# Kernel optimization log

Hardware: AMD Instinct MI355X
Metric: run time of the kernel (lower is better)

## Reference

```python
import jax, jax.numpy as jnp
import numpy as np

# Bit-slice configuration from the module defaults: slices [1,1,2,4] -> 8-bit signed INT.
# The crossbar engine's MapReduceDot decomposes the quantized integers into bit-planes,
# runs partial dot products per (input-slice, weight-slice) pair across paral_size
# partitions, and recombines them with 2^shift weights. In the ideal (noise-free)
# engine this recombination is EXACT, so the forward math equals:
#   dequant(blockwise_quant(x)) @ dequant(blockwise_quant(W^T)) + bias
# with per-block scales determined by the quant granularities.
IN_BITS = 1 + 1 + 2 + 4   # sum(input_slice)  = 8
W_BITS = 1 + 1 + 2 + 4    # sum(weight_slice) = 8
IN_GRAN = (1, 32)         # (rows, cols) blocks over (seq, in_features)
W_GRAN = (32, 32)         # blocks over (in_features, out_features) of weight.t()


def block_fake_quant(x, bits, gran):
    """Symmetric per-block fake quantization (quantize -> dequantize).

    x: [..., R, C]; gran=(gr, gc) tiles the last two dims. Each (gr, gc) block
    gets its own max-abs scale, matching SlicedData's quant_gran semantics.
    """
    qmax = float(2 ** (bits - 1) - 1)  # 127 for 8-bit
    gr, gc = gran
    lead = x.shape[:-2]
    R, C = x.shape[-2], x.shape[-1]
    xb = x.reshape(*lead, R // gr, gr, C // gc, gc)
    mx = jnp.max(jnp.abs(xb), axis=(-3, -1), keepdims=True)
    scale = jnp.where(mx > 0, mx / qmax, jnp.ones_like(mx))
    q = jnp.clip(jnp.round(xb / scale), -qmax, qmax) * scale
    return q.reshape(x.shape)


def setup_inputs() -> dict:
    key = jax.random.key(0)
    k1, k2, k3 = jax.random.split(key, 3)
    B, S, Din, Dout = 4, 4096, 2048, 2048
    x = jax.random.normal(k1, (B, S, Din), dtype=jnp.float32)
    # kaiming_uniform_(a=sqrt(5)) on a Linear weight is U(-1/sqrt(fan_in), 1/sqrt(fan_in))
    bound = 1.0 / np.sqrt(Din)
    weight = jax.random.uniform(k2, (Dout, Din), jnp.float32, -bound, bound)
    bias = jax.random.uniform(k3, (Dout,), jnp.float32, -bound, bound)
    return {"x": x, "weight": weight, "bias": bias}


def reference(x, weight, bias):
    # Quantize activations per (1, 32) block and weight.t() per (32, 32) block,
    # then recombine via the (mathematically exact) bit-sliced dot == dense GEMM
    # on the dequantized values.
    qx = block_fake_quant(x, IN_BITS, IN_GRAN)            # [B, S, Din]
    qw = block_fake_quant(weight.T, W_BITS, W_GRAN)       # [Din, Dout]
    out = jnp.einsum('bsd,de->bse', qx, qw) + bias        # [B, S, Dout]
    return out
```

## Files before the change

kernel.cpp:

```cpp
#include <hip/hip_runtime.h>
#include <hip/hip_bf16.h>
#include <stdint.h>

#define M_TOT 16384
#define N_TOT 2048
#define K_TOT 2048
#define NT 32

typedef __attribute__((ext_vector_type(8))) short bf16x8;
typedef __attribute__((ext_vector_type(4))) float f32x4;

__device__ __forceinline__ ushort f32_to_bf16_rne(float f) {
    uint32_t u = __float_as_uint(f);
    uint32_t r = (u + 0x7fffu + ((u >> 16) & 1u)) >> 16;
    return (ushort)r;
}

__device__ __forceinline__ void async_copy16(const void* gptr, void* lptr) {
    __builtin_amdgcn_global_load_lds(
        (const __attribute__((address_space(1))) uint32_t*)gptr,
        (__attribute__((address_space(3))) uint32_t*)lptr,
        16, 0, 0);
}

__global__ void quant_x_kernel(const float* __restrict__ x, ushort* __restrict__ qx) {
    const int tid = blockIdx.x * 256 + threadIdx.x;
    const float4 v = ((const float4*)x)[tid];
    float m = fmaxf(fmaxf(fabsf(v.x), fabsf(v.y)), fmaxf(fabsf(v.z), fabsf(v.w)));
    m = fmaxf(m, __shfl_xor(m, 1));
    m = fmaxf(m, __shfl_xor(m, 2));
    m = fmaxf(m, __shfl_xor(m, 4));
    const float s = (m > 0.f) ? (m / 127.f) : 1.f;
    const float q0 = fminf(fmaxf(rintf(v.x / s), -127.f), 127.f) * s;
    const float q1 = fminf(fmaxf(rintf(v.y / s), -127.f), 127.f) * s;
    const float q2 = fminf(fmaxf(rintf(v.z / s), -127.f), 127.f) * s;
    const float q3 = fminf(fmaxf(rintf(v.w / s), -127.f), 127.f) * s;
    ushort4 r;
    r.x = f32_to_bf16_rne(q0);
    r.y = f32_to_bf16_rne(q1);
    r.z = f32_to_bf16_rne(q2);
    r.w = f32_to_bf16_rne(q3);
    ((ushort4*)qx)[tid] = r;
}

__global__ void quant_w_kernel(const float* __restrict__ w, ushort* __restrict__ qw) {
    const int gtid = blockIdx.x * 256 + threadIdx.x;
    const int wid  = gtid >> 6;
    const int lane = gtid & 63;
    const int tn = wid >> 6;
    const int tk = wid & 63;
    const int row = tn * 32 + (lane >> 1);
    const int col = tk * 32 + ((lane & 1) << 4);
    const float* p = w + (size_t)row * K_TOT + col;
    const float4 v0 = ((const float4*)p)[0];
    const float4 v1 = ((const float4*)p)[1];
    const float4 v2 = ((const float4*)p)[2];
    const float4 v3 = ((const float4*)p)[3];
    float m = 0.f;
#define MAX4(V) m = fmaxf(m, fmaxf(fmaxf(fabsf(V.x), fabsf(V.y)), fmaxf(fabsf(V.z), fabsf(V.w))));
    MAX4(v0) MAX4(v1) MAX4(v2) MAX4(v3)
#undef MAX4
    #pragma unroll
    for (int off = 1; off < 64; off <<= 1) m = fmaxf(m, __shfl_xor(m, off));
    const float s = (m > 0.f) ? (m / 127.f) : 1.f;
    float vv[16] = {v0.x, v0.y, v0.z, v0.w, v1.x, v1.y, v1.z, v1.w,
                    v2.x, v2.y, v2.z, v2.w, v3.x, v3.y, v3.z, v3.w};
    union { ushort us[16]; uint4 q[2]; } o;
    #pragma unroll
    for (int i = 0; i < 16; ++i) {
        const float q = fminf(fmaxf(rintf(vv[i] / s), -127.f), 127.f) * s;
        o.us[i] = f32_to_bf16_rne(q);
    }
    uint4* dst = (uint4*)(qw + (size_t)row * K_TOT + col);
    dst[0] = o.q[0];
    dst[1] = o.q[1];
}

#define LDSA(tb, row, colus) \
    (*(const bf16x8*)&As[tb][row][(colus) ^ (((row) & 7) << 3)])
#define LDSB(slot, row, colus) \
    (*(const bf16x8*)&BsF[(size_t)(slot) * 16384 + (size_t)(row) * 64 + (((colus) ^ (((row) & 7) << 3)))])

#define STAGE_A(tb, hh, li, tt)                                                          \
    async_copy16(Agbase + (size_t)((hh) * 128 + (li) * 64) * K_TOT + (size_t)(tt) * 64,  \
                 (char*)&As[0][0][0] + (tb) * 32768 + (hh) * 16384 + (li) * 8192 + (wv << 10))
#define STAGE_B(slot, hh, li, tt)                                                        \
    async_copy16(Bgbase + (size_t)((hh) * 128 + (li) * 64) * K_TOT + (size_t)(tt) * 64,  \
                 (char*)&BsF[0] + (size_t)(slot) * 32768 + (hh) * 16384 + (li) * 8192 + (wv << 10))

#define PHASE_MFMA(i0, BGC)                                                               \
    asm volatile("s_waitcnt lgkmcnt(0)" ::: "memory");                                    \
    __builtin_amdgcn_s_setprio(1);                                                        \
    _Pragma("unroll")                                                                     \
    for (int j = 0; j < 4; ++j) {                                                         \
        acc[i0][j]     = __builtin_amdgcn_mfma_f32_16x16x32_bf16(af0, BGC[j][0], acc[i0][j], 0, 0, 0);     \
        acc[i0][j]     = __builtin_amdgcn_mfma_f32_16x16x32_bf16(af1, BGC[j][1], acc[i0][j], 0, 0, 0);     \
        acc[(i0)+1][j] = __builtin_amdgcn_mfma_f32_16x16x32_bf16(af2, BGC[j][0], acc[(i0)+1][j], 0, 0, 0); \
        acc[(i0)+1][j] = __builtin_amdgcn_mfma_f32_16x16x32_bf16(af3, BGC[j][1], acc[(i0)+1][j], 0, 0, 0); \
    }                                                                                     \
    __builtin_amdgcn_s_setprio(0);

#define TILE_BODY(tb, BGC, BGN, t)                                                        \
  {                                                                                       \
                                                                             \
    af0 = LDSA(tb, ab +  0, h8);  af1 = LDSA(tb, ab +  0, 32 + h8);                       \
    af2 = LDSA(tb, ab + 16, h8);  af3 = LDSA(tb, ab + 16, 32 + h8);                       \
    if ((t) + 1 < NT) {                                                                   \
        BGN[0][0] = LDSB(brd, bb0, h8);  BGN[0][1] = LDSB(brd, bb0, 32 + h8);             \
        STAGE_A(tb ^ 1, 0, 0, (t) + 1);  STAGE_A(tb ^ 1, 0, 1, (t) + 1);                  \
    }                                                                                     \
    PHASE_MFMA(0, BGC)                                                                    \
    __builtin_amdgcn_s_barrier();                                                         \
                                                                             \
    af0 = LDSA(tb, ab + 32, h8);  af1 = LDSA(tb, ab + 32, 32 + h8);                       \
    af2 = LDSA(tb, ab + 48, h8);  af3 = LDSA(tb, ab + 48, 32 + h8);                       \
    if ((t) + 1 < NT) {                                                                   \
        BGN[1][0] = LDSB(brd, bb1, h8);  BGN[1][1] = LDSB(brd, bb1, 32 + h8);             \
        STAGE_A(tb ^ 1, 1, 0, (t) + 1);  STAGE_A(tb ^ 1, 1, 1, (t) + 1);                  \
    }                                                                                     \
    PHASE_MFMA(2, BGC)                                                                    \
    __builtin_amdgcn_s_barrier();                                                         \
                                                                             \
    af0 = LDSA(tb, ab + 64, h8);  af1 = LDSA(tb, ab + 64, 32 + h8);                       \
    af2 = LDSA(tb, ab + 80, h8);  af3 = LDSA(tb, ab + 80, 32 + h8);                       \
    if ((t) + 1 < NT) {                                                                   \
        BGN[2][0] = LDSB(brd, bb2, h8);  BGN[2][1] = LDSB(brd, bb2, 32 + h8);             \
    }                                                                                     \
    if ((t) + 3 < NT) { STAGE_B(bwr, 0, 0, (t) + 3);  STAGE_B(bwr, 0, 1, (t) + 3); }      \
    PHASE_MFMA(4, BGC)                                                                    \
    if ((t) + 3 < NT) { asm volatile("s_waitcnt vmcnt(2)" ::: "memory"); }                \
    else              { asm volatile("s_waitcnt vmcnt(0)" ::: "memory"); }                \
    __builtin_amdgcn_s_barrier();                                                         \
                                                                             \
    af0 = LDSA(tb, ab +  96, h8);  af1 = LDSA(tb, ab +  96, 32 + h8);                     \
    af2 = LDSA(tb, ab + 112, h8);  af3 = LDSA(tb, ab + 112, 32 + h8);                     \
    if ((t) + 1 < NT) {                                                                   \
        BGN[3][0] = LDSB(brd, bb3, h8);  BGN[3][1] = LDSB(brd, bb3, 32 + h8);             \
    }                                                                                     \
    if ((t) + 3 < NT) { STAGE_B(bwr, 1, 0, (t) + 3);  STAGE_B(bwr, 1, 1, (t) + 3); }      \
    PHASE_MFMA(6, BGC)                                                                    \
    __builtin_amdgcn_s_barrier();                                                         \
  }

__global__ __launch_bounds__(512, 1) void gemm_pipe_kernel(
    const ushort* __restrict__ A,
    const ushort* __restrict__ Bt,
    const float* __restrict__ bias,
    float* __restrict__ C) {

    __shared__ ushort As[2][256][64];
    __shared__ ushort Bs[3][256][64];
    const ushort* BsF = &Bs[0][0][0];

    const int tid  = threadIdx.x;
    const int lane = tid & 63;
    const int wv   = tid >> 6;
    const int wmr  = wv >> 2;
    const int wcn  = wv & 3;
    const int r    = lane & 15;
    const int h8   = (lane >> 4) << 3;

    const int nbn  = N_TOT / 256;
    const int nwg  = (M_TOT / 256) * nbn;
    const int cpx  = nwg >> 3;
    const int swz  = (blockIdx.x & 7) * cpx + (blockIdx.x >> 3);
    const int brow = (swz / nbn) * 256;
    const int bcol = (swz % nbn) * 256;

    const int srow = tid >> 3;
    const int scol = (((tid & 7) ^ (srow & 7)) << 3);
    const ushort* Agbase = A  + (size_t)(brow + srow) * K_TOT + scol;
    const ushort* Bgbase = Bt + (size_t)(bcol + srow) * K_TOT + scol;

    const int ab  = wmr * 128 + r;
    const int bb0 = wcn * 64 +  0 + r;
    const int bb1 = wcn * 64 + 16 + r;
    const int bb2 = wcn * 64 + 32 + r;
    const int bb3 = wcn * 64 + 48 + r;

    f32x4 acc[8][4];
    const f32x4 zero = {0.f, 0.f, 0.f, 0.f};
    #pragma unroll
    for (int i = 0; i < 8; ++i)
        #pragma unroll
        for (int j = 0; j < 4; ++j) acc[i][j] = zero;

    STAGE_A(0, 0, 0, 0); STAGE_A(0, 0, 1, 0); STAGE_A(0, 1, 0, 0); STAGE_A(0, 1, 1, 0);
    STAGE_B(0, 0, 0, 0); STAGE_B(0, 0, 1, 0); STAGE_B(0, 1, 0, 0); STAGE_B(0, 1, 1, 0);
    STAGE_B(1, 0, 0, 1); STAGE_B(1, 0, 1, 1); STAGE_B(1, 1, 0, 1); STAGE_B(1, 1, 1, 1);
    asm volatile("s_waitcnt vmcnt(0)" ::: "memory");
    STAGE_B(2, 0, 0, 2); STAGE_B(2, 0, 1, 2); STAGE_B(2, 1, 0, 2); STAGE_B(2, 1, 1, 2);
    __builtin_amdgcn_s_barrier();

    bf16x8 af0, af1, af2, af3;
    bf16x8 bgA[4][2], bgB[4][2];

    bgA[0][0] = LDSB(0, bb0, h8);  bgA[0][1] = LDSB(0, bb0, 32 + h8);
    bgA[1][0] = LDSB(0, bb1, h8);  bgA[1][1] = LDSB(0, bb1, 32 + h8);
    bgA[2][0] = LDSB(0, bb2, h8);  bgA[2][1] = LDSB(0, bb2, 32 + h8);
    bgA[3][0] = LDSB(0, bb3, h8);  bgA[3][1] = LDSB(0, bb3, 32 + h8);

    int brd = 1;
    int bwr = 0;

    for (int t = 0; t < NT; t += 2) {
        TILE_BODY(0, bgA, bgB, t)
        brd = (brd == 2) ? 0 : brd + 1;  bwr = (bwr == 2) ? 0 : bwr + 1;
        TILE_BODY(1, bgB, bgA, t + 1)
        brd = (brd == 2) ? 0 : brd + 1;  bwr = (bwr == 2) ? 0 : bwr + 1;
    }

    const int hq = (lane >> 4) * 4;
    float bv[4];
    #pragma unroll
    for (int j = 0; j < 4; ++j) bv[j] = bias[bcol + wcn * 64 + j * 16 + r];
    #pragma unroll
    for (int i = 0; i < 8; ++i) {
        const int row0 = brow + wmr * 128 + i * 16 + hq;
        #pragma unroll
        for (int j = 0; j < 4; ++j) {
            const int col = bcol + wcn * 64 + j * 16 + r;
            #pragma unroll
            for (int jj = 0; jj < 4; ++jj)
                C[(size_t)(row0 + jj) * N_TOT + col] = acc[i][j][jj] + bv[j];
        }
    }
}

extern "C" void kernel_launch(void* const* d_in, const int* in_sizes, int n_in,
                              void* d_out, int out_size, void* d_ws, size_t ws_size,
                              hipStream_t stream) {
    const float* x    = (const float*)d_in[0];
    const float* wgt  = (const float*)d_in[1];
    const float* bias = (const float*)d_in[2];
    float* out = (float*)d_out;

    ushort* qx = (ushort*)d_ws;
    ushort* qw = qx + (size_t)M_TOT * K_TOT;

    quant_x_kernel<<<(M_TOT * K_TOT / 4) / 256, 256, 0, stream>>>(x, qx);
    quant_w_kernel<<<(64 * 64 * 64) / 256, 256, 0, stream>>>(wgt, qw);
    gemm_pipe_kernel<<<(M_TOT / 256) * (N_TOT / 256), 512, 0, stream>>>(qx, qw, bias, out);
}
```

Baseline: 187.1 us.

## Restructure GEMM mainloop into 8-phase schedule with double-buffered B

Replaces the triple-buffered B tile and register ping-pong of B fragments with a double-buffered B in LDS. All B fragments for a tile are now loaded from LDS at the start of each tile. The loop becomes eight barrier-separated phases, interleaving A/B global-to-LDS prefetch with MFMA blocks. This cuts LDS usage and register pressure, in exchange for a shorter B prefetch distance and twice as many barriers per tile.

Result: faster. 175.3 us (-6.3%).

```diff
diff --git a/kernel.cpp b/kernel.cpp
--- a/kernel.cpp
+++ b/kernel.cpp
@@ -78,79 +78,79 @@
 
 #define LDSA(tb, row, colus) \
     (*(const bf16x8*)&As[tb][row][(colus) ^ (((row) & 7) << 3)])
-#define LDSB(slot, row, colus) \
-    (*(const bf16x8*)&BsF[(size_t)(slot) * 16384 + (size_t)(row) * 64 + (((colus) ^ (((row) & 7) << 3)))])
+#define LDSB(tb, row, colus) \
+    (*(const bf16x8*)&Bs[tb][row][(colus) ^ (((row) & 7) << 3)])
 
 #define STAGE_A(tb, hh, li, tt)                                                          \
     async_copy16(Agbase + (size_t)((hh) * 128 + (li) * 64) * K_TOT + (size_t)(tt) * 64,  \
                  (char*)&As[0][0][0] + (tb) * 32768 + (hh) * 16384 + (li) * 8192 + (wv << 10))
-#define STAGE_B(slot, hh, li, tt)                                                        \
+#define STAGE_B(tb, hh, li, tt)                                                          \
     async_copy16(Bgbase + (size_t)((hh) * 128 + (li) * 64) * K_TOT + (size_t)(tt) * 64,  \
-                 (char*)&BsF[0] + (size_t)(slot) * 32768 + (hh) * 16384 + (li) * 8192 + (wv << 10))
-
-#define PHASE_MFMA(i0, BGC)                                                               \
+                 (char*)&Bs[0][0][0] + (tb) * 32768 + (hh) * 16384 + (li) * 8192 + (wv << 10))
+#define STAGE_A2(tb, hh, tt)  { STAGE_A(tb, hh, 0, tt); STAGE_A(tb, hh, 1, tt); }
+#define STAGE_B2(tb, hh, tt)  { STAGE_B(tb, hh, 0, tt); STAGE_B(tb, hh, 1, tt); }
+
+#define PHASE_MFMA(i0)                                                                    \
     asm volatile("s_waitcnt lgkmcnt(0)" ::: "memory");                                    \
     __builtin_amdgcn_s_setprio(1);                                                        \
     _Pragma("unroll")                                                                     \
     for (int j = 0; j < 4; ++j) {                                                         \
-        acc[i0][j]     = __builtin_amdgcn_mfma_f32_16x16x32_bf16(af0, BGC[j][0], acc[i0][j], 0, 0, 0);     \
-        acc[i0][j]     = __builtin_amdgcn_mfma_f32_16x16x32_bf16(af1, BGC[j][1], acc[i0][j], 0, 0, 0);     \
-        acc[(i0)+1][j] = __builtin_amdgcn_mfma_f32_16x16x32_bf16(af2, BGC[j][0], acc[(i0)+1][j], 0, 0, 0); \
-        acc[(i0)+1][j] = __builtin_amdgcn_mfma_f32_16x16x32_bf16(af3, BGC[j][1], acc[(i0)+1][j], 0, 0, 0); \
+        acc[i0][j]     = __builtin_amdgcn_mfma_f32_16x16x32_bf16(af0, bg[j][0], acc[i0][j], 0, 0, 0);     \
+        acc[i0][j]     = __builtin_amdgcn_mfma_f32_16x16x32_bf16(af1, bg[j][1], acc[i0][j], 0, 0, 0);     \
+        acc[(i0)+1][j] = __builtin_amdgcn_mfma_f32_16x16x32_bf16(af2, bg[j][0], acc[(i0)+1][j], 0, 0, 0); \
+        acc[(i0)+1][j] = __builtin_amdgcn_mfma_f32_16x16x32_bf16(af3, bg[j][1], acc[(i0)+1][j], 0, 0, 0); \
     }                                                                                     \
     __builtin_amdgcn_s_setprio(0);
 
-#define TILE_BODY(tb, BGC, BGN, t)                                                        \
+#define TILE_BODY(tb, t)                                                                  \
   {                                                                                       \
-                                                                             \
+    bf16x8 af0, af1, af2, af3;                                                            \
+    bf16x8 bg[4][2];                                                                      \
+                      \
     af0 = LDSA(tb, ab +  0, h8);  af1 = LDSA(tb, ab +  0, 32 + h8);                       \
     af2 = LDSA(tb, ab + 16, h8);  af3 = LDSA(tb, ab + 16, 32 + h8);                       \
-    if ((t) + 1 < NT) {                                                                   \
-        BGN[0][0] = LDSB(brd, bb0, h8);  BGN[0][1] = LDSB(brd, bb0, 32 + h8);             \
-        STAGE_A(tb ^ 1, 0, 0, (t) + 1);  STAGE_A(tb ^ 1, 0, 1, (t) + 1);                  \
-    }                                                                                     \
-    PHASE_MFMA(0, BGC)                                                                    \
-    __builtin_amdgcn_s_barrier();                                                         \
-                                                                             \
+    bg[0][0] = LDSB(tb, bb0, h8);  bg[0][1] = LDSB(tb, bb0, 32 + h8);                     \
+    bg[1][0] = LDSB(tb, bb1, h8);  bg[1][1] = LDSB(tb, bb1, 32 + h8);                     \
+    bg[2][0] = LDSB(tb, bb2, h8);  bg[2][1] = LDSB(tb, bb2, 32 + h8);                     \
+    bg[3][0] = LDSB(tb, bb3, h8);  bg[3][1] = LDSB(tb, bb3, 32 + h8);                     \
+    if ((t) + 1 < NT) STAGE_A2(tb ^ 1, 0, (t) + 1)                                        \
+    asm volatile("s_waitcnt lgkmcnt(8)" ::: "memory");                                    \
+    __builtin_amdgcn_s_barrier();                                                         \
+    PHASE_MFMA(0)                                                                         \
+    __builtin_amdgcn_s_barrier();                                                         \
+                                \
     af0 = LDSA(tb, ab + 32, h8);  af1 = LDSA(tb, ab + 32, 32 + h8);                       \
     af2 = LDSA(tb, ab + 48, h8);  af3 = LDSA(tb, ab + 48, 32 + h8);                       \
-    if ((t) + 1 < NT) {                                                                   \
-        BGN[1][0] = LDSB(brd, bb1, h8);  BGN[1][1] = LDSB(brd, bb1, 32 + h8);             \
-        STAGE_A(tb ^ 1, 1, 0, (t) + 1);  STAGE_A(tb ^ 1, 1, 1, (t) + 1);                  \
-    }                                                                                     \
-    PHASE_MFMA(2, BGC)                                                                    \
-    __builtin_amdgcn_s_barrier();                                                         \
-                                                                             \
+    if ((t) + 1 < NT) STAGE_A2(tb ^ 1, 1, (t) + 1)                                        \
+    __builtin_amdgcn_s_barrier();                                                         \
+    PHASE_MFMA(2)                                                                         \
+    __builtin_amdgcn_s_barrier();                                                         \
+           \
     af0 = LDSA(tb, ab + 64, h8);  af1 = LDSA(tb, ab + 64, 32 + h8);                       \
     af2 = LDSA(tb, ab + 80, h8);  af3 = LDSA(tb, ab + 80, 32 + h8);                       \
-    if ((t) + 1 < NT) {                                                                   \
-        BGN[2][0] = LDSB(brd, bb2, h8);  BGN[2][1] = LDSB(brd, bb2, 32 + h8);             \
-    }                                                                                     \
-    if ((t) + 3 < NT) { STAGE_B(bwr, 0, 0, (t) + 3);  STAGE_B(bwr, 0, 1, (t) + 3); }      \
-    PHASE_MFMA(4, BGC)                                                                    \
-    if ((t) + 3 < NT) { asm volatile("s_waitcnt vmcnt(2)" ::: "memory"); }                \
-    else              { asm volatile("s_waitcnt vmcnt(0)" ::: "memory"); }                \
-    __builtin_amdgcn_s_barrier();                                                         \
-                                                                             \
+    if ((t) + 2 < NT) STAGE_B2(tb, 0, (t) + 2)                                            \
+    __builtin_amdgcn_s_barrier();                                                         \
+    PHASE_MFMA(4)                                                                         \
+    __builtin_amdgcn_s_barrier();                                                         \
+                \
     af0 = LDSA(tb, ab +  96, h8);  af1 = LDSA(tb, ab +  96, 32 + h8);                     \
     af2 = LDSA(tb, ab + 112, h8);  af3 = LDSA(tb, ab + 112, 32 + h8);                     \
-    if ((t) + 1 < NT) {                                                                   \
-        BGN[3][0] = LDSB(brd, bb3, h8);  BGN[3][1] = LDSB(brd, bb3, 32 + h8);             \
-    }                                                                                     \
-    if ((t) + 3 < NT) { STAGE_B(bwr, 1, 0, (t) + 3);  STAGE_B(bwr, 1, 1, (t) + 3); }      \
-    PHASE_MFMA(6, BGC)                                                                    \
+    if ((t) + 2 < NT) STAGE_B2(tb, 1, (t) + 2)                                            \
+    __builtin_amdgcn_s_barrier();                                                         \
+    PHASE_MFMA(6)                                                                         \
+    if ((t) + 2 < NT) { asm volatile("s_waitcnt vmcnt(4)" ::: "memory"); }                \
+    else              { asm volatile("s_waitcnt vmcnt(0)" ::: "memory"); }                \
     __builtin_amdgcn_s_barrier();                                                         \
   }
 
-__global__ __launch_bounds__(512, 1) void gemm_pipe_kernel(
+__global__ __launch_bounds__(512, 1) void gemm_8ph_kernel(
     const ushort* __restrict__ A,
     const ushort* __restrict__ Bt,
     const float* __restrict__ bias,
     float* __restrict__ C) {
 
     __shared__ ushort As[2][256][64];
-    __shared__ ushort Bs[3][256][64];
-    const ushort* BsF = &Bs[0][0][0];
+    __shared__ ushort Bs[2][256][64];
 
     const int tid  = threadIdx.x;
     const int lane = tid & 63;
@@ -185,29 +185,15 @@
         #pragma unroll
         for (int j = 0; j < 4; ++j) acc[i][j] = zero;
 
-    STAGE_A(0, 0, 0, 0); STAGE_A(0, 0, 1, 0); STAGE_A(0, 1, 0, 0); STAGE_A(0, 1, 1, 0);
-    STAGE_B(0, 0, 0, 0); STAGE_B(0, 0, 1, 0); STAGE_B(0, 1, 0, 0); STAGE_B(0, 1, 1, 0);
-    STAGE_B(1, 0, 0, 1); STAGE_B(1, 0, 1, 1); STAGE_B(1, 1, 0, 1); STAGE_B(1, 1, 1, 1);
-    asm volatile("s_waitcnt vmcnt(0)" ::: "memory");
-    STAGE_B(2, 0, 0, 2); STAGE_B(2, 0, 1, 2); STAGE_B(2, 1, 0, 2); STAGE_B(2, 1, 1, 2);
+    STAGE_A2(0, 0, 0) STAGE_A2(0, 1, 0)
+    STAGE_B2(0, 0, 0) STAGE_B2(0, 1, 0)
+    STAGE_B2(1, 0, 1) STAGE_B2(1, 1, 1)
+    asm volatile("s_waitcnt vmcnt(4)" ::: "memory");
     __builtin_amdgcn_s_barrier();
 
-    bf16x8 af0, af1, af2, af3;
-    bf16x8 bgA[4][2], bgB[4][2];
-
-    bgA[0][0] = LDSB(0, bb0, h8);  bgA[0][1] = LDSB(0, bb0, 32 + h8);
-    bgA[1][0] = LDSB(0, bb1, h8);  bgA[1][1] = LDSB(0, bb1, 32 + h8);
-    bgA[2][0] = LDSB(0, bb2, h8);  bgA[2][1] = LDSB(0, bb2, 32 + h8);
-    bgA[3][0] = LDSB(0, bb3, h8);  bgA[3][1] = LDSB(0, bb3, 32 + h8);
-
-    int brd = 1;
-    int bwr = 0;
-
     for (int t = 0; t < NT; t += 2) {
-        TILE_BODY(0, bgA, bgB, t)
-        brd = (brd == 2) ? 0 : brd + 1;  bwr = (bwr == 2) ? 0 : bwr + 1;
-        TILE_BODY(1, bgB, bgA, t + 1)
-        brd = (brd == 2) ? 0 : brd + 1;  bwr = (bwr == 2) ? 0 : bwr + 1;
+        TILE_BODY(0, t)
+        TILE_BODY(1, t + 1)
     }
 
     const int hq = (lane >> 4) * 4;
@@ -240,5 +226,5 @@
 
     quant_x_kernel<<<(M_TOT * K_TOT / 4) / 256, 256, 0, stream>>>(x, qx);
     quant_w_kernel<<<(64 * 64 * 64) / 256, 256, 0, stream>>>(wgt, qw);
-    gemm_pipe_kernel<<<(M_TOT / 256) * (N_TOT / 256), 512, 0, stream>>>(qx, qw, bias, out);
-}
+    gemm_8ph_kernel<<<(M_TOT / 256) * (N_TOT / 256), 512, 0, stream>>>(qx, qw, bias, out);
+}
```
